# Optimization experiments

Hardware: AMD Instinct MI355X
Metric: run time of the kernel (lower is better)

The kernel has to match this reference:

```python
import jax, jax.numpy as jnp
import numpy as np

N_GENE, N_CT, N_REF, N_SAMPLE = 50000, 64, 16, 1024

def setup_inputs() -> dict:
    key = jax.random.key(0)
    k1, k2, k3, k4, k5, k6 = jax.random.split(key, 6)
    x = jax.random.normal(k1, (N_GENE * N_CT * N_REF,), dtype=jnp.float32)
    idx = jax.random.randint(k2, (N_CT, N_GENE), 0, N_CT * N_GENE)
    # RefCombLayer weight: uniform around 1/n_ref
    num = 1.0 / N_REF
    w_ref = jax.random.uniform(k3, (N_REF * N_CT,), minval=num - num / 5, maxval=num + num / 5, dtype=jnp.float32)
    # CelltypeScaleLayer weight: normal(1.0, 0.1)
    w_ct = 1.0 + 0.1 * jax.random.normal(k4, (N_CT,), dtype=jnp.float32)
    # StretchLayer weight: normal(1.0, 0.1)
    w_stretch = 1.0 + 0.1 * jax.random.normal(k5, (N_GENE,), dtype=jnp.float32)
    # conv1 kernel: (n_sample, 1, n_kernel), normal(1/n_ct, 0.25/n_ct)
    conv_w = (1.0 / N_CT) + (0.25 / N_CT) * jax.random.normal(k6, (N_SAMPLE, 1, N_CT), dtype=jnp.float32)
    return {"x": x, "idx": idx, "w_ref": w_ref, "w_ct": w_ct,
            "w_stretch": w_stretch, "conv_w": conv_w,
            "N_batch": 1, "N_feature": N_GENE * N_CT}


def reference(x, idx, w_ref, w_ct, w_stretch, conv_w, N_batch, N_feature):
    # RefCombLayer: elementwise mul by per-gene-tiled ref weights
    y = x * jnp.tile(w_ref, N_GENE)                       # [n_gene*n_ct*n_ref]
    # SliceSumLayer: sum over n_ref slices
    y0 = y.reshape(N_CT * N_GENE, N_REF).sum(axis=1)      # [n_ct*n_gene]
    # CelltypeScaleLayer: gather per cell type, scale, flatten transposed
    z = y0[idx] * w_ct[:, None]                           # [n_ct, n_gene]
    y1 = z.T.reshape(-1)                                  # [n_gene*n_ct], gene-major
    # StretchLayer: per-gene weight repeated n_ct times
    y2 = y1 * jnp.repeat(w_stretch, N_CT)                 # [n_gene*n_ct]
    # Conv1d(1, n_sample, kernel=n_ct, stride=n_ct) == per-gene dot with kernel
    yk = y2.reshape(N_GENE, N_CT)                         # [n_gene, n_ct]
    out = jnp.einsum('gk,sk->sg', yk, conv_w[:, 0, :])    # [n_sample, n_gene]
    return (out, y0, y1, y2)
```

## Files before the change

kernel.cpp:

```cpp
#include <hip/hip_runtime.h>

#define NG 50000
#define NCT 64
#define NREF 16
#define NS 1024
#define N0 (NCT * NG)

#define OFF_Y0 ((size_t)NS * NG)
#define OFF_Y1 (OFF_Y0 + N0)
#define OFF_Y2 (OFF_Y1 + N0)

typedef __attribute__((ext_vector_type(8))) short bf16x8;
typedef __attribute__((ext_vector_type(4))) float f32x4;

__device__ __forceinline__ unsigned short f2bf(float f) {
    union { float f; unsigned u; } v; v.f = f;
    unsigned r = v.u + 0x7fff + ((v.u >> 16) & 1);
    return (unsigned short)(r >> 16);
}
__device__ __forceinline__ float bf2f(unsigned short b) {
    union { float f; unsigned u; } v; v.u = ((unsigned)b) << 16;
    return v.f;
}

__global__ __launch_bounds__(256) void k_y0(const float* __restrict__ x,
                                            const float* __restrict__ w_ref,
                                            float* __restrict__ y0) {
    __shared__ f32x4 wl[256];
    const int tid = threadIdx.x;
    wl[tid] = reinterpret_cast<const f32x4*>(w_ref)[tid];
    __syncthreads();
    const int row = tid & 63;
    const f32x4 w0 = wl[row * 4 + 0];
    const f32x4 w1 = wl[row * 4 + 1];
    const f32x4 w2 = wl[row * 4 + 2];
    const f32x4 w3 = wl[row * 4 + 3];
    const f32x4* x4 = reinterpret_cast<const f32x4*>(x);
    const size_t stride = (size_t)gridDim.x * 256;
    for (size_t j = (size_t)blockIdx.x * 256 + tid; j < (size_t)N0; j += stride) {
        const f32x4* xp = x4 + j * 4;
        f32x4 a = __builtin_nontemporal_load(xp + 0);
        f32x4 b = __builtin_nontemporal_load(xp + 1);
        f32x4 c = __builtin_nontemporal_load(xp + 2);
        f32x4 d = __builtin_nontemporal_load(xp + 3);
        float s = a.x * w0.x + a.y * w0.y + a.z * w0.z + a.w * w0.w
                + b.x * w1.x + b.y * w1.y + b.z * w1.z + b.w * w1.w
                + c.x * w2.x + c.y * w2.y + c.z * w2.z + c.w * w2.w
                + d.x * w3.x + d.y * w3.y + d.z * w3.z + d.w * w3.w;
        y0[j] = s;
    }
}

#define STILE 128
__global__ __launch_bounds__(256) void k_fused(const float* __restrict__ y0,
                                               const int* __restrict__ idx,
                                               const float* __restrict__ w_ct,
                                               const float* __restrict__ w_stretch,
                                               const float* __restrict__ cw,
                                               float* __restrict__ y1,
                                               float* __restrict__ y2,
                                               float* __restrict__ out) {
    __shared__ unsigned short Yhi[64 * 72];
    __shared__ unsigned short Ylo[64 * 72];
    __shared__ char Rbuf[2 * STILE * 72 * 2];
    float* T = reinterpret_cast<float*>(Rbuf);
    unsigned short* Whi = reinterpret_cast<unsigned short*>(Rbuf);
    unsigned short* Wlo = Whi + STILE * 72;

    const int tid = threadIdx.x;
    const int g0 = blockIdx.x * 64;

    int ids[16];
#pragma unroll
    for (int k = 0; k < 16; ++k) {
        int lin = k * 256 + tid;
        int c = lin >> 6, gl = lin & 63;
        int gc = min(g0 + gl, NG - 1);
        ids[k] = idx[c * NG + gc];
    }
    float vals[16];
#pragma unroll
    for (int k = 0; k < 16; ++k) vals[k] = y0[ids[k]];
#pragma unroll
    for (int k = 0; k < 16; ++k) {
        int lin = k * 256 + tid;
        int c = lin >> 6, gl = lin & 63;
        T[c * 65 + gl] = vals[k];
    }
    __syncthreads();

#pragma unroll
    for (int k = 0; k < 16; ++k) {
        int lin = k * 256 + tid;
        int gl = lin >> 6, c = lin & 63;
        int g = g0 + gl;
        float t = T[c * 65 + gl];
        float v1 = t * w_ct[c];
        float v2 = v1 * w_stretch[min(g, NG - 1)];
        int base = gl * 72 + c;
        unsigned short h = f2bf(v2);
        Yhi[base] = h;
        Ylo[base] = f2bf(v2 - bf2f(h));
        if (g < NG) {
            size_t o = (size_t)g * 64 + c;
            __builtin_nontemporal_store(v1, y1 + o);
            __builtin_nontemporal_store(v2, y2 + o);
        }
    }
    __syncthreads();

    const int lane = tid & 63;
    const int wid  = tid >> 6;
    const int l15  = lane & 15;
    const int l4   = lane >> 4;
    const int nb   = wid * 32;

    bf16x8 Ah[4][2], Al[4][2];
#pragma unroll
    for (int m = 0; m < 4; ++m) {
        int grow = m * 16 + l15;
#pragma unroll
        for (int ks = 0; ks < 2; ++ks) {
            int koff = ks * 32 + l4 * 8;
            Ah[m][ks] = *reinterpret_cast<const bf16x8*>(&Yhi[grow * 72 + koff]);
            Al[m][ks] = *reinterpret_cast<const bf16x8*>(&Ylo[grow * 72 + koff]);
        }
    }

    for (int s0 = 0; s0 < NS; s0 += STILE) {
#pragma unroll
        for (int it = 0; it < 8; ++it) {
            int e0 = (it * 256 + tid) * 4;
            int sp = e0 >> 6;
            int cp = e0 & 63;
            f32x4 v = *reinterpret_cast<const f32x4*>(cw + (size_t)(s0 + sp) * 64 + cp);
            unsigned short h0 = f2bf(v.x), h1 = f2bf(v.y), h2 = f2bf(v.z), h3 = f2bf(v.w);
            int base = sp * 72 + cp;
            Whi[base + 0] = h0; Whi[base + 1] = h1; Whi[base + 2] = h2; Whi[base + 3] = h3;
            Wlo[base + 0] = f2bf(v.x - bf2f(h0));
            Wlo[base + 1] = f2bf(v.y - bf2f(h1));
            Wlo[base + 2] = f2bf(v.z - bf2f(h2));
            Wlo[base + 3] = f2bf(v.w - bf2f(h3));
        }
        __syncthreads();

        bf16x8 Bh[2][2], Bl[2][2];
#pragma unroll
        for (int n = 0; n < 2; ++n) {
            int srow = nb + n * 16 + l15;
#pragma unroll
            for (int ks = 0; ks < 2; ++ks) {
                int koff = ks * 32 + l4 * 8;
                Bh[n][ks] = *reinterpret_cast<const bf16x8*>(&Whi[srow * 72 + koff]);
                Bl[n][ks] = *reinterpret_cast<const bf16x8*>(&Wlo[srow * 72 + koff]);
            }
        }

        f32x4 acc[4][2];
#pragma unroll
        for (int m = 0; m < 4; ++m)
#pragma unroll
            for (int n = 0; n < 2; ++n) acc[m][n] = (f32x4){0.f, 0.f, 0.f, 0.f};

#pragma unroll
        for (int m = 0; m < 4; ++m)
#pragma unroll
            for (int n = 0; n < 2; ++n)
#pragma unroll
                for (int ks = 0; ks < 2; ++ks) {
                    acc[m][n] = __builtin_amdgcn_mfma_f32_16x16x32_bf16(Ah[m][ks], Bh[n][ks], acc[m][n], 0, 0, 0);
                    acc[m][n] = __builtin_amdgcn_mfma_f32_16x16x32_bf16(Ah[m][ks], Bl[n][ks], acc[m][n], 0, 0, 0);
                    acc[m][n] = __builtin_amdgcn_mfma_f32_16x16x32_bf16(Al[m][ks], Bh[n][ks], acc[m][n], 0, 0, 0);
                }

#pragma unroll
        for (int m = 0; m < 4; ++m) {
            int g4 = g0 + m * 16 + l4 * 4;
            if (g4 < NG) {
#pragma unroll
                for (int n = 0; n < 2; ++n) {
                    int s = s0 + nb + n * 16 + l15;
                    __builtin_nontemporal_store(acc[m][n], reinterpret_cast<f32x4*>(out + (size_t)s * NG + g4));
                }
            }
        }
        __syncthreads();
    }
}

extern "C" void kernel_launch(void* const* d_in, const int* in_sizes, int n_in,
                              void* d_out, int out_size, void* d_ws, size_t ws_size,
                              hipStream_t stream) {
    const float* x         = (const float*)d_in[0];
    const int*   idx       = (const int*)d_in[1];
    const float* w_ref     = (const float*)d_in[2];
    const float* w_ct      = (const float*)d_in[3];
    const float* w_stretch = (const float*)d_in[4];
    const float* conv_w    = (const float*)d_in[5];

    float* out = (float*)d_out;
    float* y0  = out + OFF_Y0;
    float* y1  = out + OFF_Y1;
    float* y2  = out + OFF_Y2;

    k_y0<<<2048, 256, 0, stream>>>(x, w_ref, y0);
    k_fused<<<(NG + 63) / 64, 256, 0, stream>>>(y0, idx, w_ct, w_stretch, conv_w, y1, y2, out);
}
```

Before: 180.2 us.

## Load conv weights directly from global memory, pre-split to bf16 hi/lo in workspace

Removes the per-tile LDS staging of conv weights and the two block barriers per sample tile; each wave now loads its B fragments straight from global memory, served by L2 since the weights are shared. When workspace is large enough, a small pre-kernel converts conv_w once into bf16 hi/lo arrays, so the fused kernel no longer repeats the conversion in every block. Otherwise each wave converts its own fragments in registers. The cost is more global/L2 traffic per block and an extra kernel launch.

```diff
diff --git a/kernel.cpp b/kernel.cpp
--- a/kernel.cpp
+++ b/kernel.cpp
@@ -12,6 +12,7 @@
 
 typedef __attribute__((ext_vector_type(8))) short bf16x8;
 typedef __attribute__((ext_vector_type(4))) float f32x4;
+typedef __attribute__((ext_vector_type(4))) unsigned short u16x4;
 
 __device__ __forceinline__ unsigned short f2bf(float f) {
     union { float f; unsigned u; } v; v.f = f;
@@ -51,21 +52,37 @@
     }
 }
 
+__global__ __launch_bounds__(256) void k_cw(const float* __restrict__ cw,
+                                            unsigned short* __restrict__ cwhi,
+                                            unsigned short* __restrict__ cwlo) {
+    int i = (blockIdx.x * 256 + threadIdx.x) * 4;
+    f32x4 v = *reinterpret_cast<const f32x4*>(cw + i);
+    u16x4 h, l;
+#pragma unroll
+    for (int e = 0; e < 4; ++e) {
+        unsigned short hh = f2bf(v[e]);
+        h[e] = hh;
+        l[e] = f2bf(v[e] - bf2f(hh));
+    }
+    *reinterpret_cast<u16x4*>(cwhi + i) = h;
+    *reinterpret_cast<u16x4*>(cwlo + i) = l;
+}
+
 #define STILE 128
+template<bool PRECONV>
 __global__ __launch_bounds__(256) void k_fused(const float* __restrict__ y0,
                                                const int* __restrict__ idx,
                                                const float* __restrict__ w_ct,
                                                const float* __restrict__ w_stretch,
                                                const float* __restrict__ cw,
+                                               const unsigned short* __restrict__ cwhi,
+                                               const unsigned short* __restrict__ cwlo,
                                                float* __restrict__ y1,
                                                float* __restrict__ y2,
                                                float* __restrict__ out) {
+    __shared__ float T[64 * 65];
     __shared__ unsigned short Yhi[64 * 72];
     __shared__ unsigned short Ylo[64 * 72];
-    __shared__ char Rbuf[2 * STILE * 72 * 2];
-    float* T = reinterpret_cast<float*>(Rbuf);
-    unsigned short* Whi = reinterpret_cast<unsigned short*>(Rbuf);
-    unsigned short* Wlo = Whi + STILE * 72;
 
     const int tid = threadIdx.x;
     const int g0 = blockIdx.x * 64;
@@ -128,50 +145,45 @@
     }
 
     for (int s0 = 0; s0 < NS; s0 += STILE) {
-#pragma unroll
-        for (int it = 0; it < 8; ++it) {
-            int e0 = (it * 256 + tid) * 4;
-            int sp = e0 >> 6;
-            int cp = e0 & 63;
-            f32x4 v = *reinterpret_cast<const f32x4*>(cw + (size_t)(s0 + sp) * 64 + cp);
-            unsigned short h0 = f2bf(v.x), h1 = f2bf(v.y), h2 = f2bf(v.z), h3 = f2bf(v.w);
-            int base = sp * 72 + cp;
-            Whi[base + 0] = h0; Whi[base + 1] = h1; Whi[base + 2] = h2; Whi[base + 3] = h3;
-            Wlo[base + 0] = f2bf(v.x - bf2f(h0));
-            Wlo[base + 1] = f2bf(v.y - bf2f(h1));
-            Wlo[base + 2] = f2bf(v.z - bf2f(h2));
-            Wlo[base + 3] = f2bf(v.w - bf2f(h3));
-        }
-        __syncthreads();
-
-        bf16x8 Bh[2][2], Bl[2][2];
+        f32x4 acc[4][2];
+#pragma unroll
+        for (int m = 0; m < 4; ++m)
+#pragma unroll
+            for (int n = 0; n < 2; ++n) acc[m][n] = (f32x4){0.f, 0.f, 0.f, 0.f};
+
 #pragma unroll
         for (int n = 0; n < 2; ++n) {
-            int srow = nb + n * 16 + l15;
+            const size_t srow = (size_t)(s0 + nb + n * 16 + l15) * 64;
+            bf16x8 Bh[2], Bl[2];
 #pragma unroll
             for (int ks = 0; ks < 2; ++ks) {
                 int koff = ks * 32 + l4 * 8;
-                Bh[n][ks] = *reinterpret_cast<const bf16x8*>(&Whi[srow * 72 + koff]);
-                Bl[n][ks] = *reinterpret_cast<const bf16x8*>(&Wlo[srow * 72 + koff]);
+                if (PRECONV) {
+                    Bh[ks] = *reinterpret_cast<const bf16x8*>(cwhi + srow + koff);
+                    Bl[ks] = *reinterpret_cast<const bf16x8*>(cwlo + srow + koff);
+                } else {
+                    f32x4 va = *reinterpret_cast<const f32x4*>(cw + srow + koff);
+                    f32x4 vb = *reinterpret_cast<const f32x4*>(cw + srow + koff + 4);
+#pragma unroll
+                    for (int e = 0; e < 4; ++e) {
+                        unsigned short h = f2bf(va[e]);
+                        Bh[ks][e] = (short)h;
+                        Bl[ks][e] = (short)f2bf(va[e] - bf2f(h));
+                        h = f2bf(vb[e]);
+                        Bh[ks][e + 4] = (short)h;
+                        Bl[ks][e + 4] = (short)f2bf(vb[e] - bf2f(h));
+                    }
+                }
             }
-        }
-
-        f32x4 acc[4][2];
-#pragma unroll
-        for (int m = 0; m < 4; ++m)
-#pragma unroll
-            for (int n = 0; n < 2; ++n) acc[m][n] = (f32x4){0.f, 0.f, 0.f, 0.f};
-
-#pragma unroll
-        for (int m = 0; m < 4; ++m)
-#pragma unroll
-            for (int n = 0; n < 2; ++n)
+#pragma unroll
+            for (int m = 0; m < 4; ++m)
 #pragma unroll
                 for (int ks = 0; ks < 2; ++ks) {
-                    acc[m][n] = __builtin_amdgcn_mfma_f32_16x16x32_bf16(Ah[m][ks], Bh[n][ks], acc[m][n], 0, 0, 0);
-                    acc[m][n] = __builtin_amdgcn_mfma_f32_16x16x32_bf16(Ah[m][ks], Bl[n][ks], acc[m][n], 0, 0, 0);
-                    acc[m][n] = __builtin_amdgcn_mfma_f32_16x16x32_bf16(Al[m][ks], Bh[n][ks], acc[m][n], 0, 0, 0);
+                    acc[m][n] = __builtin_amdgcn_mfma_f32_16x16x32_bf16(Ah[m][ks], Bh[ks], acc[m][n], 0, 0, 0);
+                    acc[m][n] = __builtin_amdgcn_mfma_f32_16x16x32_bf16(Ah[m][ks], Bl[ks], acc[m][n], 0, 0, 0);
+                    acc[m][n] = __builtin_amdgcn_mfma_f32_16x16x32_bf16(Al[m][ks], Bh[ks], acc[m][n], 0, 0, 0);
                 }
+        }
 
 #pragma unroll
         for (int m = 0; m < 4; ++m) {
@@ -184,7 +196,6 @@
                 }
             }
         }
-        __syncthreads();
     }
 }
 
@@ -204,5 +215,16 @@
     float* y2  = out + OFF_Y2;
 
     k_y0<<<2048, 256, 0, stream>>>(x, w_ref, y0);
-    k_fused<<<(NG + 63) / 64, 256, 0, stream>>>(y0, idx, w_ct, w_stretch, conv_w, y1, y2, out);
-}
+
+    const bool preconv = (ws_size >= (size_t)NS * NCT * 2 * sizeof(unsigned short));
+    unsigned short* cwhi = (unsigned short*)d_ws;
+    unsigned short* cwlo = cwhi + NS * NCT;
+    if (preconv) {
+        k_cw<<<NS * NCT / 1024, 256, 0, stream>>>(conv_w, cwhi, cwlo);
+        k_fused<true><<<(NG + 63) / 64, 256, 0, stream>>>(y0, idx, w_ct, w_stretch, conv_w,
+                                                          cwhi, cwlo, y1, y2, out);
+    } else {
+        k_fused<false><<<(NG + 63) / 64, 256, 0, stream>>>(y0, idx, w_ct, w_stretch, conv_w,
+                                                           cwhi, cwlo, y1, y2, out);
+    }
+}
```

After: 187.4 us. +4.0%, slower.
